# Optimization experiments

Measured on AMD Instinct MI355X. Metric: run time of the kernel, lower is better.

## Reference

```python
import jax, jax.numpy as jnp
import numpy as np

D_MODEL = 1024
NUM_HEADS = 16
HEAD_DIM = D_MODEL // NUM_HEADS


def setup_inputs() -> dict:
    key = jax.random.key(0)
    ks = jax.random.split(key, 5)
    x = jax.random.normal(ks[0], (2, 2048, D_MODEL), dtype=jnp.float32)
    # torch nn.Linear init scale ~ U(-1/sqrt(in), 1/sqrt(in)); use small normals
    s = 1.0 / np.sqrt(D_MODEL)
    W_qkv = jax.random.normal(ks[1], (D_MODEL, 3 * D_MODEL), dtype=jnp.float32) * s
    b_qkv = jax.random.normal(ks[2], (3 * D_MODEL,), dtype=jnp.float32) * s
    W_out = jax.random.normal(ks[3], (D_MODEL, D_MODEL), dtype=jnp.float32) * s
    b_out = jax.random.normal(ks[4], (D_MODEL,), dtype=jnp.float32) * s
    return {"x": x, "W_qkv": W_qkv, "b_qkv": b_qkv, "W_out": W_out, "b_out": b_out}


def reference(x, W_qkv, b_qkv, W_out, b_out):
    B, S, _ = x.shape
    qkv = x @ W_qkv + b_qkv                                  # [B,S,3D]
    qkv = qkv.reshape(B, S, NUM_HEADS, 3 * HEAD_DIM).transpose(0, 2, 1, 3)  # [B,H,S,3d]
    q, k, v = jnp.split(qkv, 3, axis=-1)                     # each [B,H,S,d]
    scale = 1.0 / np.sqrt(HEAD_DIM)
    scores = jnp.einsum("bhqd,bhkd->bhqk", q, k) * scale      # [B,H,S,S]
    attn = jax.nn.softmax(scores, axis=-1)
    values = jnp.einsum("bhqk,bhkd->bhqd", attn, v)           # [B,H,S,d]
    values = values.transpose(0, 2, 1, 3).reshape(B, S, D_MODEL)
    return values @ W_out + b_out
```

## Files before the change

kernel.cpp:

```cpp
#include <hip/hip_runtime.h>


#define D_MODEL 1024
#define NHEAD   16
#define HDIM    64
#define SEQ     2048
#define BATCH   2
#define NTOK    (BATCH * SEQ)

typedef float    f32x4  __attribute__((ext_vector_type(4)));
typedef float    f32x16 __attribute__((ext_vector_type(16)));
typedef _Float16 f16x8  __attribute__((ext_vector_type(8)));
typedef _Float16 f16x4  __attribute__((ext_vector_type(4)));

#define GLOBAL_LOAD_LDS16(gptr, lptr)                                            \
    __builtin_amdgcn_global_load_lds(                                            \
        (const __attribute__((address_space(1))) unsigned int*)(gptr),           \
        (__attribute__((address_space(3))) unsigned int*)(lptr), 16, 0, 0)

__global__ __launch_bounds__(256) void prep_kernel(
    const float* __restrict__ x, _Float16* __restrict__ xh,
    const float* __restrict__ Wqkv, _Float16* __restrict__ wq_t,
    const float* __restrict__ Wout, _Float16* __restrict__ wo_t)
{
    const int bx = blockIdx.x;
    const int tid = threadIdx.x;
    if (bx < 4096) {
        const int i = (bx * 256 + tid) * 4;
        const float4 v = *(const float4*)&x[i];
        f16x4 hh;
        hh[0] = (_Float16)v.x; hh[1] = (_Float16)v.y;
        hh[2] = (_Float16)v.z; hh[3] = (_Float16)v.w;
        *(f16x4*)&xh[i] = hh;
        return;
    }
    __shared__ float ts[64][65];
    const float* W; _Float16* Wt; int N, n0, k0;
    if (bx < 4096 + 768) {
        const int local = bx - 4096;
        W = Wqkv; Wt = wq_t; N = 3072;
        n0 = (local % 48) * 64; k0 = (local / 48) * 64;
    } else {
        const int local = bx - 4864;
        W = Wout; Wt = wo_t; N = 1024;
        n0 = (local % 16) * 64; k0 = (local / 16) * 64;
    }
    {
        const int r = tid >> 2, c = (tid & 3) << 4;
        const float* src = W + (size_t)(k0 + r) * N + n0 + c;
        #pragma unroll
        for (int u = 0; u < 4; ++u)
            *(float4*)&ts[r][c + u * 4] = *(const float4*)&src[u * 4];
    }
    __syncthreads();
    {
        const int n = tid >> 2, kg = (tid & 3) << 4;
        f16x8 v0, v1;
        #pragma unroll
        for (int j = 0; j < 8; ++j) {
            v0[j] = (_Float16)ts[kg + j][n];
            v1[j] = (_Float16)ts[kg + 8 + j][n];
        }
        _Float16* dst = Wt + (size_t)(n0 + n) * D_MODEL + k0 + kg;
        *(f16x8*)&dst[0] = v0;
        *(f16x8*)&dst[8] = v1;
    }
}

__global__ __launch_bounds__(512) void gemm_qkv_kernel(
    const _Float16* __restrict__ A, const _Float16* __restrict__ Bt,
    const float* __restrict__ bias, _Float16* __restrict__ Cout,
    int M, int N, int K)
{
    __shared__ _Float16 lds[2][4096];
    const int tid = threadIdx.x;
    const int wave = tid >> 6, lane = tid & 63;
    const int quad = lane >> 4, l16 = lane & 15;
    const int m0 = blockIdx.y * 128, n0 = blockIdx.x * 128;
    const int wr = wave >> 1, wc = wave & 1;

    f32x4 acc[2][4] = {};

    const bool isA = wave < 4;
    const _Float16* gsrc = isA ? (A + (size_t)m0 * K) : (Bt + (size_t)n0 * K);
    _Float16* ldst = isA ? &lds[0][0] : &lds[1][0];
    const int sbase = (wave & 3) * 2;

    for (int k0 = 0; k0 < K; k0 += 32) {
        __syncthreads();
        #pragma unroll
        for (int j = 0; j < 2; ++j) {
            const int seg = sbase + j;
            const int chunk = seg >> 1;
            const int row = ((seg & 1) << 6) | lane;
            GLOBAL_LOAD_LDS16(gsrc + (size_t)row * K + k0 + chunk * 8, ldst + seg * 512);
        }
        __syncthreads();

        f16x8 a[2], b[4];
        #pragma unroll
        for (int mt = 0; mt < 2; ++mt)
            a[mt] = *(const f16x8*)&lds[0][quad * 1024 + (wr * 32 + mt * 16 + l16) * 8];
        #pragma unroll
        for (int nt = 0; nt < 4; ++nt)
            b[nt] = *(const f16x8*)&lds[1][quad * 1024 + (wc * 64 + nt * 16 + l16) * 8];
        #pragma unroll
        for (int mt = 0; mt < 2; ++mt)
            #pragma unroll
            for (int nt = 0; nt < 4; ++nt)
                acc[mt][nt] = __builtin_amdgcn_mfma_f32_16x16x32_f16(a[mt], b[nt], acc[mt][nt], 0, 0, 0);
    }

    #pragma unroll
    for (int nt = 0; nt < 4; ++nt) {
        const int col = n0 + wc * 64 + nt * 16 + l16;
        const float bv = bias[col];
        #pragma unroll
        for (int mt = 0; mt < 2; ++mt) {
            #pragma unroll
            for (int r = 0; r < 4; ++r) {
                const int row = m0 + wr * 32 + mt * 16 + quad * 4 + r;
                Cout[(size_t)row * N + col] = (_Float16)(acc[mt][nt][r] + bv);
            }
        }
    }
}

__global__ __launch_bounds__(512) void gemm_out_kernel(
    const _Float16* __restrict__ A, const _Float16* __restrict__ Bt,
    const float* __restrict__ bias, float* __restrict__ Cout)
{
    const int K = D_MODEL, N = D_MODEL;
    __shared__ _Float16 ldsA[4096];
    __shared__ _Float16 ldsB[2048];
    const int tid = threadIdx.x;
    const int wave = tid >> 6, lane = tid & 63;
    const int quad = lane >> 4, l16 = lane & 15;
    const int m0 = blockIdx.y * 128, n0 = blockIdx.x * 64;
    const int wr = wave >> 1, wc = wave & 1;

    f32x4 acc[2][2] = {};

    for (int k0 = 0; k0 < K; k0 += 32) {
        __syncthreads();
        if (wave < 4) {
            #pragma unroll
            for (int j = 0; j < 2; ++j) {
                const int seg = wave * 2 + j;
                const int chunk = seg >> 1;
                const int row = ((seg & 1) << 6) | lane;
                GLOBAL_LOAD_LDS16(A + (size_t)(m0 + row) * K + k0 + chunk * 8, ldsA + seg * 512);
            }
        } else {
            const int seg = wave - 4;
            GLOBAL_LOAD_LDS16(Bt + (size_t)(n0 + lane) * K + k0 + seg * 8, ldsB + seg * 512);
        }
        __syncthreads();

        f16x8 a[2], b[2];
        #pragma unroll
        for (int mt = 0; mt < 2; ++mt)
            a[mt] = *(const f16x8*)&ldsA[quad * 1024 + (wr * 32 + mt * 16 + l16) * 8];
        #pragma unroll
        for (int nt = 0; nt < 2; ++nt)
            b[nt] = *(const f16x8*)&ldsB[quad * 512 + (wc * 32 + nt * 16 + l16) * 8];
        #pragma unroll
        for (int mt = 0; mt < 2; ++mt)
            #pragma unroll
            for (int nt = 0; nt < 2; ++nt)
                acc[mt][nt] = __builtin_amdgcn_mfma_f32_16x16x32_f16(a[mt], b[nt], acc[mt][nt], 0, 0, 0);
    }

    #pragma unroll
    for (int nt = 0; nt < 2; ++nt) {
        const int col = n0 + wc * 32 + nt * 16 + l16;
        const float bv = bias[col];
        #pragma unroll
        for (int mt = 0; mt < 2; ++mt) {
            #pragma unroll
            for (int r = 0; r < 4; ++r) {
                const int row = m0 + wr * 32 + mt * 16 + quad * 4 + r;
                Cout[(size_t)row * N + col] = acc[mt][nt][r] + bv;
            }
        }
    }
}

__global__ __launch_bounds__(256) void swizzle_kv_kernel(
    const _Float16* __restrict__ qkv,
    _Float16* __restrict__ Ksw, _Float16* __restrict__ Vsw)
{
    __shared__ _Float16 ts[64][72];
    const int tid = threadIdx.x;
    const int s0 = blockIdx.x * 64, h = blockIdx.y, b = blockIdx.z;
    const size_t hsz = (size_t)8 * SEQ * 8;
    _Float16* kh = Ksw + (size_t)(b * NHEAD + h) * hsz;
    _Float16* vh = Vsw + (size_t)(b * NHEAD + h) * hsz;

    {
        const int s = s0 + (tid >> 2);
        const int dg = (tid & 3) << 4;
        const _Float16* src = qkv + (size_t)(b * SEQ + s) * (3 * D_MODEL) + h * (3 * HDIM) + HDIM + dg;
        const f16x8 v0 = *(const f16x8*)&src[0];
        const f16x8 v1 = *(const f16x8*)&src[8];
        const int c0 = dg >> 3;
        *(f16x8*)&kh[((size_t)c0 * SEQ + s) * 8]       = v0;
        *(f16x8*)&kh[((size_t)(c0 + 1) * SEQ + s) * 8] = v1;
    }
    {
        const int s = tid >> 2, dg = (tid & 3) << 4;
        const _Float16* src = qkv + (size_t)(b * SEQ + s0 + s) * (3 * D_MODEL) + h * (3 * HDIM) + 2 * HDIM + dg;
        *(f16x8*)&ts[s][dg]     = *(const f16x8*)&src[0];
        *(f16x8*)&ts[s][dg + 8] = *(const f16x8*)&src[8];
    }
    __syncthreads();
    {
        const int d = tid >> 2, sg = (tid & 3) << 4;
        f16x8 v0, v1;
        #pragma unroll
        for (int j = 0; j < 8; ++j) { v0[j] = ts[sg + j][d]; v1[j] = ts[sg + 8 + j][d]; }
        const int cs0 = (s0 + sg) >> 3;
        *(f16x8*)&vh[((size_t)cs0 * HDIM + d) * 8]       = v0;
        *(f16x8*)&vh[((size_t)(cs0 + 1) * HDIM + d) * 8] = v1;
    }
}

__global__ __launch_bounds__(256) void attn_mfma_kernel(
    const _Float16* __restrict__ qkv,
    const _Float16* __restrict__ Ksw, const _Float16* __restrict__ Vsw,
    _Float16* __restrict__ val)
{
    __shared__ _Float16 Ks[2][4096];
    __shared__ _Float16 Vts[2][4096];
    __shared__ _Float16 Ps[128 * 72];

    const int tid = threadIdx.x;
    const int wave = tid >> 6, lane = tid & 63;
    const int l31 = lane & 31, hi = lane >> 5;
    const int qt = blockIdx.x, h = blockIdx.y, b = blockIdx.z;
    const int q0 = qt * 128;

    const size_t hsz = (size_t)8 * SEQ * 8;
    const _Float16* kh = Ksw + (size_t)(b * NHEAD + h) * hsz;
    const _Float16* vh = Vsw + (size_t)(b * NHEAD + h) * hsz;

    f16x8 qf[4];
    {
        const int row = q0 + wave * 32 + l31;
        const _Float16* src = qkv + (size_t)(b * SEQ + row) * (3 * D_MODEL) + h * (3 * HDIM) + hi * 8;
        #pragma unroll
        for (int kk = 0; kk < 4; ++kk) {
            const f16x8 t = *(const f16x8*)(src + kk * 16);
            #pragma unroll
            for (int j = 0; j < 8; ++j)
                qf[kk][j] = (_Float16)((float)t[j] * 0.1803368802f);
        }
    }

    f32x16 acc0 = {};
    f32x16 acc1 = {};
    float rs = 0.f;

    _Float16* const psrow = &Ps[(wave * 32 + l31) * 72];

    #pragma unroll
    for (int jj = 0; jj < 2; ++jj) {
        const int c = wave * 2 + jj;
        GLOBAL_LOAD_LDS16(kh + ((size_t)c * SEQ + lane) * 8, &Ks[0][c * 512]);
        GLOBAL_LOAD_LDS16(vh + ((size_t)c * HDIM + lane) * 8, &Vts[0][c * 512]);
    }
    __syncthreads();

    for (int kt = 0; kt < SEQ / 64; ++kt) {
        const int cur = kt & 1;

        if (kt + 1 < SEQ / 64) {
            #pragma unroll
            for (int jj = 0; jj < 2; ++jj) {
                const int c = wave * 2 + jj;
                GLOBAL_LOAD_LDS16(kh + ((size_t)c * SEQ + (kt + 1) * 64 + lane) * 8,
                                  &Ks[cur ^ 1][c * 512]);
                GLOBAL_LOAD_LDS16(vh + ((size_t)((kt + 1) * 8 + c) * HDIM + lane) * 8,
                                  &Vts[cur ^ 1][c * 512]);
            }
        }

        f32x16 s0 = {};
        f32x16 s1 = {};
        #pragma unroll
        for (int kk = 0; kk < 4; ++kk) {
            const f16x8 k0 = *(const f16x8*)&Ks[cur][(kk * 2 + hi) * 512 + l31 * 8];
            const f16x8 k1 = *(const f16x8*)&Ks[cur][(kk * 2 + hi) * 512 + (32 + l31) * 8];
            s0 = __builtin_amdgcn_mfma_f32_32x32x16_f16(k0, qf[kk], s0, 0, 0, 0);
            s1 = __builtin_amdgcn_mfma_f32_32x32x16_f16(k1, qf[kk], s1, 0, 0, 0);
        }

        #pragma unroll
        for (int rg = 0; rg < 4; ++rg) {
            const float p0 = __builtin_amdgcn_exp2f(s0[rg * 4 + 0]);
            const float p1 = __builtin_amdgcn_exp2f(s0[rg * 4 + 1]);
            const float p2 = __builtin_amdgcn_exp2f(s0[rg * 4 + 2]);
            const float p3 = __builtin_amdgcn_exp2f(s0[rg * 4 + 3]);
            rs += (p0 + p1) + (p2 + p3);
            uint2 w;
            w.x = __builtin_bit_cast(unsigned, __builtin_amdgcn_cvt_pkrtz(p0, p1));
            w.y = __builtin_bit_cast(unsigned, __builtin_amdgcn_cvt_pkrtz(p2, p3));
            *(uint2*)&psrow[rg * 8 + hi * 4] = w;
        }
        #pragma unroll
        for (int rg = 0; rg < 4; ++rg) {
            const float p0 = __builtin_amdgcn_exp2f(s1[rg * 4 + 0]);
            const float p1 = __builtin_amdgcn_exp2f(s1[rg * 4 + 1]);
            const float p2 = __builtin_amdgcn_exp2f(s1[rg * 4 + 2]);
            const float p3 = __builtin_amdgcn_exp2f(s1[rg * 4 + 3]);
            rs += (p0 + p1) + (p2 + p3);
            uint2 w;
            w.x = __builtin_bit_cast(unsigned, __builtin_amdgcn_cvt_pkrtz(p0, p1));
            w.y = __builtin_bit_cast(unsigned, __builtin_amdgcn_cvt_pkrtz(p2, p3));
            *(uint2*)&psrow[32 + rg * 8 + hi * 4] = w;
        }

        #pragma unroll
        for (int ks = 0; ks < 4; ++ks) {
            const f16x8 pa = *(const f16x8*)&psrow[ks * 16 + hi * 8];
            const f16x8 v0 = *(const f16x8*)&Vts[cur][(ks * 2 + hi) * 512 + l31 * 8];
            const f16x8 v1 = *(const f16x8*)&Vts[cur][(ks * 2 + hi) * 512 + (32 + l31) * 8];
            acc0 = __builtin_amdgcn_mfma_f32_32x32x16_f16(pa, v0, acc0, 0, 0, 0);
            acc1 = __builtin_amdgcn_mfma_f32_32x32x16_f16(pa, v1, acc1, 0, 0, 0);
        }

        __syncthreads();
    }

    rs += __shfl_xor(rs, 32);
    const float inv = 1.f / rs;

    #pragma unroll
    for (int r = 0; r < 16; ++r) {
        const int qo = (r & 3) + 8 * (r >> 2) + 4 * hi;
        const float invr = __shfl(inv, qo);
        const int row = b * SEQ + q0 + wave * 32 + qo;
        val[(size_t)row * D_MODEL + h * HDIM + l31]      = (_Float16)(acc0[r] * invr);
        val[(size_t)row * D_MODEL + h * HDIM + 32 + l31] = (_Float16)(acc1[r] * invr);
    }
}

extern "C" void kernel_launch(void* const* d_in, const int* in_sizes, int n_in,
                              void* d_out, int out_size, void* d_ws, size_t ws_size,
                              hipStream_t stream)
{
    const float* x     = (const float*)d_in[0];
    const float* W_qkv = (const float*)d_in[1];
    const float* b_qkv = (const float*)d_in[2];
    const float* W_out = (const float*)d_in[3];
    const float* b_out = (const float*)d_in[4];

    char* ws = (char*)d_ws;
    _Float16* Ksw   = (_Float16*)ws;
    _Float16* val_h = (_Float16*)(ws + (8u << 20));
    _Float16* wq_t  = (_Float16*)(ws + (16u << 20));
    _Float16* wo_t  = (_Float16*)(ws + (22u << 20));
    _Float16* qkv_h = (_Float16*)(ws + (24u << 20));
    _Float16* x_h   = (_Float16*)(ws + (48u << 20));
    _Float16* Vsw   = (_Float16*)(ws + (48u << 20));

    prep_kernel<<<5120, 256, 0, stream>>>(x, x_h, W_qkv, wq_t, W_out, wo_t);
    gemm_qkv_kernel<<<dim3(3 * D_MODEL / 128, NTOK / 128), 512, 0, stream>>>(
        x_h, wq_t, b_qkv, qkv_h, NTOK, 3 * D_MODEL, D_MODEL);
    swizzle_kv_kernel<<<dim3(SEQ / 64, NHEAD, BATCH), 256, 0, stream>>>(qkv_h, Ksw, Vsw);
    attn_mfma_kernel<<<dim3(SEQ / 128, NHEAD, BATCH), 256, 0, stream>>>(qkv_h, Ksw, Vsw, val_h);
    gemm_out_kernel<<<dim3(D_MODEL / 64, NTOK / 128), 512, 0, stream>>>(
        val_h, wo_t, b_out, (float*)d_out);
}
```

Baseline: 226.8 us.

## Keep softmax probabilities in registers via permlane32 swap, remap blocks per XCD, add setprio

The P tile no longer goes through LDS. Probabilities are packed to fp16 and rearranged across the lane halves with permlane32_swap so they can feed the PV MFMA directly as A operands. This removes an LDS write/read round trip per tile and frees LDS, which may allow more resident blocks. Blocks are also remapped with a 1D grid so that consecutive blocks on each XCD share the same (b,h) K/V for L2 reuse. s_setprio is raised around the MFMA sections.

Measured after the change: 223.7 us. Within noise of the previous version (-1.4%).

```diff
diff --git a/kernel.cpp b/kernel.cpp
--- a/kernel.cpp
+++ b/kernel.cpp
@@ -232,12 +232,15 @@
 {
     __shared__ _Float16 Ks[2][4096];
     __shared__ _Float16 Vts[2][4096];
-    __shared__ _Float16 Ps[128 * 72];
 
     const int tid = threadIdx.x;
     const int wave = tid >> 6, lane = tid & 63;
     const int l31 = lane & 31, hi = lane >> 5;
-    const int qt = blockIdx.x, h = blockIdx.y, b = blockIdx.z;
+
+    const int id = blockIdx.x;
+    const int g  = (id & 7) * 64 + (id >> 3);
+    const int qt = g & 15, hb = g >> 4;
+    const int h  = hb & 15, b = hb >> 4;
     const int q0 = qt * 128;
 
     const size_t hsz = (size_t)8 * SEQ * 8;
@@ -260,8 +263,6 @@
     f32x16 acc0 = {};
     f32x16 acc1 = {};
     float rs = 0.f;
-
-    _Float16* const psrow = &Ps[(wave * 32 + l31) * 72];
 
     #pragma unroll
     for (int jj = 0; jj < 2; ++jj) {
@@ -287,6 +288,7 @@
 
         f32x16 s0 = {};
         f32x16 s1 = {};
+        __builtin_amdgcn_s_setprio(1);
         #pragma unroll
         for (int kk = 0; kk < 4; ++kk) {
             const f16x8 k0 = *(const f16x8*)&Ks[cur][(kk * 2 + hi) * 512 + l31 * 8];
@@ -294,40 +296,52 @@
             s0 = __builtin_amdgcn_mfma_f32_32x32x16_f16(k0, qf[kk], s0, 0, 0, 0);
             s1 = __builtin_amdgcn_mfma_f32_32x32x16_f16(k1, qf[kk], s1, 0, 0, 0);
         }
-
-        #pragma unroll
-        for (int rg = 0; rg < 4; ++rg) {
-            const float p0 = __builtin_amdgcn_exp2f(s0[rg * 4 + 0]);
-            const float p1 = __builtin_amdgcn_exp2f(s0[rg * 4 + 1]);
-            const float p2 = __builtin_amdgcn_exp2f(s0[rg * 4 + 2]);
-            const float p3 = __builtin_amdgcn_exp2f(s0[rg * 4 + 3]);
-            rs += (p0 + p1) + (p2 + p3);
-            uint2 w;
-            w.x = __builtin_bit_cast(unsigned, __builtin_amdgcn_cvt_pkrtz(p0, p1));
-            w.y = __builtin_bit_cast(unsigned, __builtin_amdgcn_cvt_pkrtz(p2, p3));
-            *(uint2*)&psrow[rg * 8 + hi * 4] = w;
-        }
-        #pragma unroll
-        for (int rg = 0; rg < 4; ++rg) {
-            const float p0 = __builtin_amdgcn_exp2f(s1[rg * 4 + 0]);
-            const float p1 = __builtin_amdgcn_exp2f(s1[rg * 4 + 1]);
-            const float p2 = __builtin_amdgcn_exp2f(s1[rg * 4 + 2]);
-            const float p3 = __builtin_amdgcn_exp2f(s1[rg * 4 + 3]);
-            rs += (p0 + p1) + (p2 + p3);
-            uint2 w;
-            w.x = __builtin_bit_cast(unsigned, __builtin_amdgcn_cvt_pkrtz(p0, p1));
-            w.y = __builtin_bit_cast(unsigned, __builtin_amdgcn_cvt_pkrtz(p2, p3));
-            *(uint2*)&psrow[32 + rg * 8 + hi * 4] = w;
-        }
-
+        __builtin_amdgcn_s_setprio(0);
+
+        f16x8 pa[4];
+        #pragma unroll
+        for (int half = 0; half < 2; ++half) {
+            const f32x16 sv = half ? s1 : s0;
+            float p[16];
+            #pragma unroll
+            for (int r = 0; r < 16; ++r)
+                p[r] = __builtin_amdgcn_exp2f(sv[r]);
+            #pragma unroll
+            for (int r = 0; r < 16; r += 4)
+                rs += (p[r] + p[r + 1]) + (p[r + 2] + p[r + 3]);
+
+            union { f16x8 h; unsigned u[4]; } lo, hh;
+            {
+                const unsigned A = __builtin_bit_cast(unsigned, __builtin_amdgcn_cvt_pkrtz(p[0], p[1]));
+                const unsigned B = __builtin_bit_cast(unsigned, __builtin_amdgcn_cvt_pkrtz(p[2], p[3]));
+                const unsigned C = __builtin_bit_cast(unsigned, __builtin_amdgcn_cvt_pkrtz(p[4], p[5]));
+                const unsigned D = __builtin_bit_cast(unsigned, __builtin_amdgcn_cvt_pkrtz(p[6], p[7]));
+                const auto rac = __builtin_amdgcn_permlane32_swap(A, C, false, false);
+                const auto rbd = __builtin_amdgcn_permlane32_swap(B, D, false, false);
+                lo.u[0] = rac[0]; lo.u[1] = rbd[0]; lo.u[2] = rac[1]; lo.u[3] = rbd[1];
+            }
+            {
+                const unsigned E = __builtin_bit_cast(unsigned, __builtin_amdgcn_cvt_pkrtz(p[8],  p[9]));
+                const unsigned F = __builtin_bit_cast(unsigned, __builtin_amdgcn_cvt_pkrtz(p[10], p[11]));
+                const unsigned G = __builtin_bit_cast(unsigned, __builtin_amdgcn_cvt_pkrtz(p[12], p[13]));
+                const unsigned H = __builtin_bit_cast(unsigned, __builtin_amdgcn_cvt_pkrtz(p[14], p[15]));
+                const auto reg = __builtin_amdgcn_permlane32_swap(E, G, false, false);
+                const auto rfh = __builtin_amdgcn_permlane32_swap(F, H, false, false);
+                hh.u[0] = reg[0]; hh.u[1] = rfh[0]; hh.u[2] = reg[1]; hh.u[3] = rfh[1];
+            }
+            pa[half * 2]     = lo.h;
+            pa[half * 2 + 1] = hh.h;
+        }
+
+        __builtin_amdgcn_s_setprio(1);
         #pragma unroll
         for (int ks = 0; ks < 4; ++ks) {
-            const f16x8 pa = *(const f16x8*)&psrow[ks * 16 + hi * 8];
             const f16x8 v0 = *(const f16x8*)&Vts[cur][(ks * 2 + hi) * 512 + l31 * 8];
             const f16x8 v1 = *(const f16x8*)&Vts[cur][(ks * 2 + hi) * 512 + (32 + l31) * 8];
-            acc0 = __builtin_amdgcn_mfma_f32_32x32x16_f16(pa, v0, acc0, 0, 0, 0);
-            acc1 = __builtin_amdgcn_mfma_f32_32x32x16_f16(pa, v1, acc1, 0, 0, 0);
-        }
+            acc0 = __builtin_amdgcn_mfma_f32_32x32x16_f16(pa[ks], v0, acc0, 0, 0, 0);
+            acc1 = __builtin_amdgcn_mfma_f32_32x32x16_f16(pa[ks], v1, acc1, 0, 0, 0);
+        }
+        __builtin_amdgcn_s_setprio(0);
 
         __syncthreads();
     }
@@ -368,7 +382,7 @@
     gemm_qkv_kernel<<<dim3(3 * D_MODEL / 128, NTOK / 128), 512, 0, stream>>>(
         x_h, wq_t, b_qkv, qkv_h, NTOK, 3 * D_MODEL, D_MODEL);
     swizzle_kv_kernel<<<dim3(SEQ / 64, NHEAD, BATCH), 256, 0, stream>>>(qkv_h, Ksw, Vsw);
-    attn_mfma_kernel<<<dim3(SEQ / 128, NHEAD, BATCH), 256, 0, stream>>>(qkv_h, Ksw, Vsw, val_h);
+    attn_mfma_kernel<<<dim3(512, 1, 1), 256, 0, stream>>>(qkv_h, Ksw, Vsw, val_h);
     gemm_out_kernel<<<dim3(D_MODEL / 64, NTOK / 128), 512, 0, stream>>>(
         val_h, wo_t, b_out, (float*)d_out);
 }
```
